# Performance work log

Hardware: AMD Instinct MI355X
Metric: run time of the kernel (lower is better)

The kernel has to match this reference:

```python
import jax, jax.numpy as jnp
import numpy as np

ROWS, COLS, BATCH, NC, DEG = 256, 512, 512, 5, 16
N = (ROWS + COLS) * BATCH            # total nodes
E = ROWS * DEG * BATCH               # total edges
EPS = 1e-07

def _idx_sets():
    blk = np.arange(BATCH)[:, None] * (ROWS + COLS)
    idx_check = (blk + np.arange(ROWS)[None, :]).ravel()          # index_one
    idx_var = (blk + ROWS + np.arange(COLS)[None, :]).ravel()      # index_two
    return jnp.asarray(idx_check, jnp.int32), jnp.asarray(idx_var, jnp.int32)

IDX_CHECK, IDX_VAR = _idx_sets()

def setup_inputs() -> dict:
    key = jax.random.key(0)
    ks = jax.random.split(key, 18)
    rng = np.random.default_rng(0)
    # per-graph block offsets; row0 = check node ids, row1 = variable ids BEFORE the +ROWS shift
    offs = np.repeat(np.arange(BATCH) * (ROWS + COLS), ROWS * DEG)
    src = offs + rng.integers(0, ROWS, size=E)
    dst = offs + rng.integers(0, COLS, size=E)
    edge_index = jnp.asarray(np.stack([src, dst]), jnp.int32)
    x = jax.random.normal(ks[0], (N, 1), jnp.float32)

    def p(k, shape, fan):
        return (jax.random.uniform(k, shape, jnp.float32) * 2.0 - 1.0) / np.sqrt(fan)

    inp = {"x": x, "edge_index": edge_index}
    for li, base in ((1, 1), (2, 9)):
        inp[f"w1_{li}"] = p(ks[base + 0], (10, 2), 2)
        inp[f"b1_{li}"] = p(ks[base + 1], (10,), 2)
        inp[f"w2_{li}"] = p(ks[base + 2], (1, 10), 10)
        inp[f"b2_{li}"] = p(ks[base + 3], (1,), 10)
        inp[f"wih_{li}"] = p(ks[base + 4], (3, 1), 1)
        inp[f"whh_{li}"] = p(ks[base + 5], (3, 1), 1)
        inp[f"bih_{li}"] = p(ks[base + 6], (3,), 1)
        inp[f"bhh_{li}"] = p(ks[base + 7], (3,), 1)
    return inp

def _ggc(h, j_idx, i_idx, agg_idx, upd_idx, w1, b1, w2, b2, wih, whh, bih, bhh):
    # message: mlp(cat[x_j, x_i])
    feat = jnp.concatenate([h[j_idx], h[i_idx]], axis=1)          # [E,2]
    hid = jax.nn.relu(feat @ w1.T + b1)                            # [E,10]
    msg = hid @ w2.T + b2                                          # [E,1]
    m = jax.ops.segment_sum(msg, agg_idx, num_segments=N)          # scatter-add -> [N,1]
    # GRUCell(input=h[idx], hx=m[idx])   (note: original passes old state as INPUT, message as HIDDEN)
    xg = h[upd_idx]
    hx = m[upd_idx]
    gi = xg @ wih.T + bih                                          # [K,3]
    gh = hx @ whh.T + bhh                                          # [K,3]
    r = jax.nn.sigmoid(gi[:, 0:1] + gh[:, 0:1])
    z = jax.nn.sigmoid(gi[:, 1:2] + gh[:, 1:2])
    n = jnp.tanh(gi[:, 2:3] + r * gh[:, 2:3])
    hnew = (1.0 - z) * n + z * hx
    return h.at[upd_idx].set(hnew)

def reference(x, edge_index, w1_1, b1_1, w2_1, b2_1, wih_1, whh_1, bih_1, bhh_1,
              w1_2, b1_2, w2_2, b2_2, wih_2, whh_2, bih_2, bhh_2):
    src = edge_index[0]
    dst = edge_index[1] + ROWS          # shift variable ids into node index space
    h = x
    for _ in range(NC):
        # ggc1: source_to_target -> x_j=h[src], x_i=h[dst], aggregate at dst, update variable nodes
        h = _ggc(h, src, dst, dst, IDX_VAR, w1_1, b1_1, w2_1, b2_1, wih_1, whh_1, bih_1, bhh_1)
        # ggc2: target_to_source -> x_j=h[dst], x_i=h[src], aggregate at src, update check nodes
        h = _ggc(h, dst, src, src, IDX_CHECK, w1_2, b1_2, w2_2, b2_2, wih_2, whh_2, bih_2, bhh_2)
    return jnp.clip(jax.nn.sigmoid(-h), EPS, 1.0 - EPS)
```

## Files before the change

### kernel.cpp

```cpp
#include <hip/hip_runtime.h>

#define ROWS 256
#define COLS 512
#define BATCH 512
#define NC 5
#define DEG 16
#define EPG (ROWS * DEG)
#define NPG (ROWS + COLS)
#define NT 512
#define EPT (EPG / NT)
#define EPSF 1e-7f

typedef unsigned short u16;
typedef unsigned int   u32;
typedef float v2f __attribute__((ext_vector_type(2)));

__device__ __forceinline__ float sigmoid_f(float a) {
    return 1.0f / (1.0f + __expf(-a));
}
__device__ __forceinline__ float tanh_f(float a) {
    return fmaf(2.0f, 1.0f / (1.0f + __expf(-2.0f * a)), -1.0f);
}

__global__ __launch_bounds__(NT, 4) void gnni_kernel(
    const float* __restrict__ x,
    const int*   __restrict__ eidx,
    const float* __restrict__ w1_1, const float* __restrict__ b1_1,
    const float* __restrict__ w2_1, const float* __restrict__ b2_1,
    const float* __restrict__ wih_1, const float* __restrict__ whh_1,
    const float* __restrict__ bih_1, const float* __restrict__ bhh_1,
    const float* __restrict__ w1_2, const float* __restrict__ b1_2,
    const float* __restrict__ w2_2, const float* __restrict__ b2_2,
    const float* __restrict__ wih_2, const float* __restrict__ whh_2,
    const float* __restrict__ bih_2, const float* __restrict__ bhh_2,
    float* __restrict__ out)
{
    __shared__ float msg[EPG];
    __shared__ u32  cntd[COLS];
    __shared__ u32  cnts[ROWS];
    __shared__ u16  ofs_v[COLS + 1];
    __shared__ u16  ofs_c[ROWS + 1];
    __shared__ float hc[ROWS];
    __shared__ float hv[COLS];
    __shared__ u32  wsum[8];
    __shared__ u32  wsum2[4];

    const int tid  = threadIdx.x;
    const int lane = tid & 63;
    const int wid  = tid >> 6;
    const int b    = blockIdx.x;
    const int base = b * NPG;
    const long ebase = (long)b * EPG;

    const int4 sa = *(const int4*)(eidx + ebase + tid * 8);
    const int4 sb = *(const int4*)(eidx + ebase + tid * 8 + 4);
    const int4 da = *(const int4*)(eidx + (long)BATCH * EPG + ebase + tid * 8);
    const int4 db = *(const int4*)(eidx + (long)BATCH * EPG + ebase + tid * 8 + 4);
    const int sarr[EPT] = {sa.x, sa.y, sa.z, sa.w, sb.x, sb.y, sb.z, sb.w};
    const int darr[EPT] = {da.x, da.y, da.z, da.w, db.x, db.y, db.z, db.w};
    u32 ep[EPT];
    #pragma unroll
    for (int i = 0; i < EPT; ++i)
        ep[i] = (u32)(sarr[i] - base) | ((u32)(darr[i] - base) << 16);

    if (tid < COLS) cntd[tid] = 0;
    if (tid < ROWS) cnts[tid] = 0;
    __syncthreads();
    #pragma unroll
    for (int i = 0; i < EPT; ++i) {
        atomicAdd(&cntd[ep[i] >> 16], 1u);
        atomicAdd(&cnts[ep[i] & 0xffffu], 1u);
    }
    __syncthreads();

    u32 myd = cntd[tid];
    u32 scv = myd;
    #pragma unroll
    for (int st = 1; st < 64; st <<= 1) {
        u32 t = __shfl_up(scv, st);
        if (lane >= st) scv += t;
    }
    if (lane == 63) wsum[wid] = scv;
    u32 mys = 0, scc = 0;
    if (tid < ROWS) {
        mys = cnts[tid];
        scc = mys;
        #pragma unroll
        for (int st = 1; st < 64; st <<= 1) {
            u32 t = __shfl_up(scc, st);
            if (lane >= st) scc += t;
        }
        if (lane == 63) wsum2[wid] = scc;
    }
    __syncthreads();
    if (tid < 8) {
        u32 v = wsum[tid];
        #pragma unroll
        for (int st = 1; st < 8; st <<= 1) {
            u32 t = __shfl_up(v, st);
            if (tid >= st) v += t;
        }
        wsum[tid] = v;
    } else if (tid < 12) {
        u32 v = wsum2[tid - 8];
        #pragma unroll
        for (int st = 1; st < 4; st <<= 1) {
            u32 t = __shfl_up(v, st);
            if (tid - 8 >= st) v += t;
        }
        wsum2[tid - 8] = v;
    }
    __syncthreads();

    {
        u32 inc = scv + (wid ? wsum[wid - 1] : 0u);
        ofs_v[tid + 1] = (u16)inc;
        if (tid == 0) ofs_v[0] = 0;
        cntd[tid] = inc - myd;
    }
    if (tid < ROWS) {
        u32 inc = scc + (wid ? wsum2[wid - 1] : 0u);
        ofs_c[tid + 1] = (u16)inc;
        if (tid == 0) ofs_c[0] = 0;
        cnts[tid] = inc - mys;
        hc[tid] = x[base + tid];
    }
    float hvreg = x[base + ROWS + tid];
    hv[tid] = hvreg;
    __syncthreads();

    u32 pos1[EPT], pos2[EPT];
    #pragma unroll
    for (int i = 0; i < EPT; ++i) {
        pos1[i] = atomicAdd(&cntd[ep[i] >> 16], 1u);
        pos2[i] = atomicAdd(&cnts[ep[i] & 0xffffu], 1u);
    }

    v2f A1[5], C1[5], B1[5], W1[5], A2[5], C2[5], B2[5], W2[5];
    #pragma unroll
    for (int j = 0; j < 5; ++j) {
        A1[j] = (v2f){w1_1[4*j],     w1_1[4*j + 2]};
        C1[j] = (v2f){w1_1[4*j + 1], w1_1[4*j + 3]};
        B1[j] = (v2f){b1_1[2*j],     b1_1[2*j + 1]};
        W1[j] = (v2f){w2_1[2*j],     w2_1[2*j + 1]};
        A2[j] = (v2f){w1_2[4*j],     w1_2[4*j + 2]};
        C2[j] = (v2f){w1_2[4*j + 1], w1_2[4*j + 3]};
        B2[j] = (v2f){b1_2[2*j],     b1_2[2*j + 1]};
        W2[j] = (v2f){w2_2[2*j],     w2_2[2*j + 1]};
    }
    const float b2_1s = b2_1[0], b2_2s = b2_2[0];
    const v2f zero2 = (v2f){0.0f, 0.0f};

    for (int it = 0; it < NC; ++it) {
        #pragma unroll
        for (int i = 0; i < EPT; ++i) {
            const u32 p = ep[i];
            const float xj = hc[p & 0xffffu];
            const float xi = hv[p >> 16];
            const v2f xj2 = (v2f){xj, xj}, xi2 = (v2f){xi, xi};
            v2f acc = (v2f){b2_1s, 0.0f};
            #pragma unroll
            for (int j = 0; j < 5; ++j) {
                v2f t = __builtin_elementwise_fma(C1[j], xi2, B1[j]);
                t = __builtin_elementwise_fma(A1[j], xj2, t);
                t = __builtin_elementwise_max(t, zero2);
                acc = __builtin_elementwise_fma(W1[j], t, acc);
            }
            msg[pos1[i]] = acc.x + acc.y;
        }
        __syncthreads();

        {
            const int beg = ofs_v[tid], end = ofs_v[tid + 1];
            float hx = 0.0f;
            for (int e = beg; e < end; ++e) hx += msg[e];
            const float xg = hvreg;
            float gi0 = fmaf(wih_1[0], xg, bih_1[0]);
            float gi1 = fmaf(wih_1[1], xg, bih_1[1]);
            float gi2 = fmaf(wih_1[2], xg, bih_1[2]);
            float gh0 = fmaf(whh_1[0], hx, bhh_1[0]);
            float gh1 = fmaf(whh_1[1], hx, bhh_1[1]);
            float gh2 = fmaf(whh_1[2], hx, bhh_1[2]);
            float r = sigmoid_f(gi0 + gh0);
            float z = sigmoid_f(gi1 + gh1);
            float n = tanh_f(fmaf(r, gh2, gi2));
            hvreg = fmaf(1.0f - z, n, z * hx);
            hv[tid] = hvreg;
        }
        __syncthreads();

        #pragma unroll
        for (int i = 0; i < EPT; ++i) {
            const u32 p = ep[i];
            const float xi = hc[p & 0xffffu];
            const float xj = hv[p >> 16];
            const v2f xj2 = (v2f){xj, xj}, xi2 = (v2f){xi, xi};
            v2f acc = (v2f){b2_2s, 0.0f};
            #pragma unroll
            for (int j = 0; j < 5; ++j) {
                v2f t = __builtin_elementwise_fma(C2[j], xi2, B2[j]);
                t = __builtin_elementwise_fma(A2[j], xj2, t);
                t = __builtin_elementwise_max(t, zero2);
                acc = __builtin_elementwise_fma(W2[j], t, acc);
            }
            msg[pos2[i]] = acc.x + acc.y;
        }
        __syncthreads();

        {
            const int c    = tid >> 1;
            const int half = tid & 1;
            const int beg = ofs_c[c], end = ofs_c[c + 1];
            const int h0  = (end - beg + 1) >> 1;
            const int lo  = half ? (beg + h0) : beg;
            const int hi  = half ? end : (beg + h0);
            float part = 0.0f;
            for (int e = lo; e < hi; ++e) part += msg[e];
            part += __shfl_xor(part, 1);
            if (half == 0) {
                const float hx = part;
                const float xg = hc[c];
                float gi0 = fmaf(wih_2[0], xg, bih_2[0]);
                float gi1 = fmaf(wih_2[1], xg, bih_2[1]);
                float gi2 = fmaf(wih_2[2], xg, bih_2[2]);
                float gh0 = fmaf(whh_2[0], hx, bhh_2[0]);
                float gh1 = fmaf(whh_2[1], hx, bhh_2[1]);
                float gh2 = fmaf(whh_2[2], hx, bhh_2[2]);
                float r = sigmoid_f(gi0 + gh0);
                float z = sigmoid_f(gi1 + gh1);
                float n = tanh_f(fmaf(r, gh2, gi2));
                hc[c] = fmaf(1.0f - z, n, z * hx);
            }
        }
        __syncthreads();
    }

    {
        float sgm = 1.0f / (1.0f + __expf(hvreg));
        out[base + ROWS + tid] = fminf(fmaxf(sgm, EPSF), 1.0f - EPSF);
    }
    if (tid < ROWS) {
        float sgm = 1.0f / (1.0f + __expf(hc[tid]));
        out[base + tid] = fminf(fmaxf(sgm, EPSF), 1.0f - EPSF);
    }
}

extern "C" void kernel_launch(void* const* d_in, const int* in_sizes, int n_in,
                              void* d_out, int out_size, void* d_ws, size_t ws_size,
                              hipStream_t stream) {
    const float* x    = (const float*)d_in[0];
    const int*   eidx = (const int*)d_in[1];
    gnni_kernel<<<BATCH, NT, 0, stream>>>(
        x, eidx,
        (const float*)d_in[2],  (const float*)d_in[3],
        (const float*)d_in[4],  (const float*)d_in[5],
        (const float*)d_in[6],  (const float*)d_in[7],
        (const float*)d_in[8],  (const float*)d_in[9],
        (const float*)d_in[10], (const float*)d_in[11],
        (const float*)d_in[12], (const float*)d_in[13],
        (const float*)d_in[14], (const float*)d_in[15],
        (const float*)d_in[16], (const float*)d_in[17],
        (float*)d_out);
}
```

Before: 40.65 us.

## Sort edges by destination in shared memory and reduce runs with LDS atomics

Edges are counting-sorted once into two shared arrays, one ordered by destination and one by source. Each thread then processes 8 consecutive edges, accumulates a running sum while the target node stays the same, and flushes it with a shared-memory float atomicAdd. This replaces the per-edge message buffer and the CSR segment-sum loops, so the variable-side and check-side reductions no longer need a separate gather pass over msg. The cost is float atomics whose summation order varies between runs, extra LDS use for two 16 KB edge arrays, and reads of hv/hc that become less coalesced after sorting.

```diff
diff --git a/kernel.cpp b/kernel.cpp
--- a/kernel.cpp
+++ b/kernel.cpp
@@ -11,8 +11,7 @@
 #define EPT (EPG / NT)
 #define EPSF 1e-7f
 
-typedef unsigned short u16;
-typedef unsigned int   u32;
+typedef unsigned int u32;
 typedef float v2f __attribute__((ext_vector_type(2)));
 
 __device__ __forceinline__ float sigmoid_f(float a) {
@@ -35,11 +34,12 @@
     const float* __restrict__ bih_2, const float* __restrict__ bhh_2,
     float* __restrict__ out)
 {
-    __shared__ float msg[EPG];
+    __shared__ u32  e1[EPG];
+    __shared__ u32  e2[EPG];
     __shared__ u32  cntd[COLS];
     __shared__ u32  cnts[ROWS];
-    __shared__ u16  ofs_v[COLS + 1];
-    __shared__ u16  ofs_c[ROWS + 1];
+    __shared__ float mv[COLS];
+    __shared__ float mc[ROWS];
     __shared__ float hc[ROWS];
     __shared__ float hv[COLS];
     __shared__ u32  wsum[8];
@@ -63,9 +63,11 @@
     for (int i = 0; i < EPT; ++i)
         ep[i] = (u32)(sarr[i] - base) | ((u32)(darr[i] - base) << 16);
 
-    if (tid < COLS) cntd[tid] = 0;
-    if (tid < ROWS) cnts[tid] = 0;
-    __syncthreads();
+    cntd[tid] = 0;
+    mv[tid] = 0.0f;
+    if (tid < ROWS) { cnts[tid] = 0; mc[tid] = 0.0f; }
+    __syncthreads();
+
     #pragma unroll
     for (int i = 0; i < EPT; ++i) {
         atomicAdd(&cntd[ep[i] >> 16], 1u);
@@ -111,29 +113,30 @@
         wsum2[tid - 8] = v;
     }
     __syncthreads();
-
-    {
-        u32 inc = scv + (wid ? wsum[wid - 1] : 0u);
-        ofs_v[tid + 1] = (u16)inc;
-        if (tid == 0) ofs_v[0] = 0;
-        cntd[tid] = inc - myd;
-    }
+    cntd[tid] = scv + (wid ? wsum[wid - 1] : 0u) - myd;
     if (tid < ROWS) {
-        u32 inc = scc + (wid ? wsum2[wid - 1] : 0u);
-        ofs_c[tid + 1] = (u16)inc;
-        if (tid == 0) ofs_c[0] = 0;
-        cnts[tid] = inc - mys;
+        cnts[tid] = scc + (wid ? wsum2[wid - 1] : 0u) - mys;
         hc[tid] = x[base + tid];
     }
     float hvreg = x[base + ROWS + tid];
     hv[tid] = hvreg;
     __syncthreads();
 
-    u32 pos1[EPT], pos2[EPT];
     #pragma unroll
     for (int i = 0; i < EPT; ++i) {
-        pos1[i] = atomicAdd(&cntd[ep[i] >> 16], 1u);
-        pos2[i] = atomicAdd(&cnts[ep[i] & 0xffffu], 1u);
+        u32 p = ep[i];
+        u32 pos = atomicAdd(&cntd[p >> 16], 1u);
+        e1[pos] = p;
+        u32 pos2 = atomicAdd(&cnts[p & 0xffffu], 1u);
+        e2[pos2] = p;
+    }
+    __syncthreads();
+
+    u32 eq1[EPT], eq2[EPT];
+    #pragma unroll
+    for (int i = 0; i < EPT; ++i) {
+        eq1[i] = e1[tid * 8 + i];
+        eq2[i] = e2[tid * 8 + i];
     }
 
     v2f A1[5], C1[5], B1[5], W1[5], A2[5], C2[5], B2[5], W2[5];
@@ -152,28 +155,38 @@
     const v2f zero2 = (v2f){0.0f, 0.0f};
 
     for (int it = 0; it < NC; ++it) {
-        #pragma unroll
-        for (int i = 0; i < EPT; ++i) {
-            const u32 p = ep[i];
-            const float xj = hc[p & 0xffffu];
-            const float xi = hv[p >> 16];
-            const v2f xj2 = (v2f){xj, xj}, xi2 = (v2f){xi, xi};
-            v2f acc = (v2f){b2_1s, 0.0f};
+        {
+            int curd = (int)(eq1[0] >> 16);
+            float xi = hv[curd];
+            float run = 0.0f;
             #pragma unroll
-            for (int j = 0; j < 5; ++j) {
-                v2f t = __builtin_elementwise_fma(C1[j], xi2, B1[j]);
-                t = __builtin_elementwise_fma(A1[j], xj2, t);
-                t = __builtin_elementwise_max(t, zero2);
-                acc = __builtin_elementwise_fma(W1[j], t, acc);
+            for (int i = 0; i < EPT; ++i) {
+                const u32 p = eq1[i];
+                const int d = (int)(p >> 16);
+                const int s = (int)(p & 0xffffu);
+                if (d != curd) {
+                    atomicAdd(&mv[curd], run);
+                    run = 0.0f; curd = d; xi = hv[d];
+                }
+                const float xj = hc[s];
+                const v2f xj2 = (v2f){xj, xj}, xi2 = (v2f){xi, xi};
+                v2f acc = (v2f){b2_1s, 0.0f};
+                #pragma unroll
+                for (int j = 0; j < 5; ++j) {
+                    v2f t = __builtin_elementwise_fma(C1[j], xi2, B1[j]);
+                    t = __builtin_elementwise_fma(A1[j], xj2, t);
+                    t = __builtin_elementwise_max(t, zero2);
+                    acc = __builtin_elementwise_fma(W1[j], t, acc);
+                }
+                run += acc.x + acc.y;
             }
-            msg[pos1[i]] = acc.x + acc.y;
+            atomicAdd(&mv[curd], run);
         }
         __syncthreads();
 
         {
-            const int beg = ofs_v[tid], end = ofs_v[tid + 1];
-            float hx = 0.0f;
-            for (int e = beg; e < end; ++e) hx += msg[e];
+            const float hx = mv[tid];
+            mv[tid] = 0.0f;
             const float xg = hvreg;
             float gi0 = fmaf(wih_1[0], xg, bih_1[0]);
             float gi1 = fmaf(wih_1[1], xg, bih_1[1]);
@@ -189,48 +202,49 @@
         }
         __syncthreads();
 
-        #pragma unroll
-        for (int i = 0; i < EPT; ++i) {
-            const u32 p = ep[i];
-            const float xi = hc[p & 0xffffu];
-            const float xj = hv[p >> 16];
-            const v2f xj2 = (v2f){xj, xj}, xi2 = (v2f){xi, xi};
-            v2f acc = (v2f){b2_2s, 0.0f};
+        {
+            int curs = (int)(eq2[0] & 0xffffu);
+            float xi = hc[curs];
+            float run = 0.0f;
             #pragma unroll
-            for (int j = 0; j < 5; ++j) {
-                v2f t = __builtin_elementwise_fma(C2[j], xi2, B2[j]);
-                t = __builtin_elementwise_fma(A2[j], xj2, t);
-                t = __builtin_elementwise_max(t, zero2);
-                acc = __builtin_elementwise_fma(W2[j], t, acc);
+            for (int i = 0; i < EPT; ++i) {
+                const u32 p = eq2[i];
+                const int s = (int)(p & 0xffffu);
+                const int d = (int)(p >> 16);
+                if (s != curs) {
+                    atomicAdd(&mc[curs], run);
+                    run = 0.0f; curs = s; xi = hc[s];
+                }
+                const float xj = hv[d];
+                const v2f xj2 = (v2f){xj, xj}, xi2 = (v2f){xi, xi};
+                v2f acc = (v2f){b2_2s, 0.0f};
+                #pragma unroll
+                for (int j = 0; j < 5; ++j) {
+                    v2f t = __builtin_elementwise_fma(C2[j], xi2, B2[j]);
+                    t = __builtin_elementwise_fma(A2[j], xj2, t);
+                    t = __builtin_elementwise_max(t, zero2);
+                    acc = __builtin_elementwise_fma(W2[j], t, acc);
+                }
+                run += acc.x + acc.y;
             }
-            msg[pos2[i]] = acc.x + acc.y;
-        }
-        __syncthreads();
-
-        {
-            const int c    = tid >> 1;
-            const int half = tid & 1;
-            const int beg = ofs_c[c], end = ofs_c[c + 1];
-            const int h0  = (end - beg + 1) >> 1;
-            const int lo  = half ? (beg + h0) : beg;
-            const int hi  = half ? end : (beg + h0);
-            float part = 0.0f;
-            for (int e = lo; e < hi; ++e) part += msg[e];
-            part += __shfl_xor(part, 1);
-            if (half == 0) {
-                const float hx = part;
-                const float xg = hc[c];
-                float gi0 = fmaf(wih_2[0], xg, bih_2[0]);
-                float gi1 = fmaf(wih_2[1], xg, bih_2[1]);
-                float gi2 = fmaf(wih_2[2], xg, bih_2[2]);
-                float gh0 = fmaf(whh_2[0], hx, bhh_2[0]);
-                float gh1 = fmaf(whh_2[1], hx, bhh_2[1]);
-                float gh2 = fmaf(whh_2[2], hx, bhh_2[2]);
-                float r = sigmoid_f(gi0 + gh0);
-                float z = sigmoid_f(gi1 + gh1);
-                float n = tanh_f(fmaf(r, gh2, gi2));
-                hc[c] = fmaf(1.0f - z, n, z * hx);
-            }
+            atomicAdd(&mc[curs], run);
+        }
+        __syncthreads();
+
+        if (tid < ROWS) {
+            const float hx = mc[tid];
+            mc[tid] = 0.0f;
+            const float xg = hc[tid];
+            float gi0 = fmaf(wih_2[0], xg, bih_2[0]);
+            float gi1 = fmaf(wih_2[1], xg, bih_2[1]);
+            float gi2 = fmaf(wih_2[2], xg, bih_2[2]);
+            float gh0 = fmaf(whh_2[0], hx, bhh_2[0]);
+            float gh1 = fmaf(whh_2[1], hx, bhh_2[1]);
+            float gh2 = fmaf(whh_2[2], hx, bhh_2[2]);
+            float r = sigmoid_f(gi0 + gh0);
+            float z = sigmoid_f(gi1 + gh1);
+            float n = tanh_f(fmaf(r, gh2, gi2));
+            hc[tid] = fmaf(1.0f - z, n, z * hx);
         }
         __syncthreads();
     }
```

Result: slower. 55.93 us (+37.6%).
